# Optimization experiments

Hardware: AMD Instinct MI355X
Metric: run time of the kernel (lower is better)

## Reference

```python
import jax, jax.numpy as jnp
import numpy as np


def setup_inputs() -> dict:
    key = jax.random.key(0)
    ks = jax.random.split(key, 5)
    B, T, in_dim, out_dim = 8, 1024, 4096, 4096
    b_in, b_out, bs_in, bs_out, rank = 16, 16, 256, 256, 128
    std = np.sqrt(0.02).astype(np.float32)
    x = jax.random.normal(ks[0], (B, T, in_dim), dtype=jnp.float32)
    S = jax.random.uniform(ks[1], (b_out, b_in, rank), dtype=jnp.float32)
    U = std * jax.random.normal(ks[2], (b_out, rank, bs_out), dtype=jnp.float32)
    Vt = std * jax.random.normal(ks[3], (b_in, bs_in, rank), dtype=jnp.float32)
    bias = jax.random.normal(ks[4], (out_dim,), dtype=jnp.float32)
    return {"x": x, "S": S, "U": U, "Vt": Vt, "bias": bias}


def _blast_weight(S, U, Vt, in_dim):
    # Faithful to AbstractBlast.weight(eye(in_dim)): pass identity through the
    # block low-rank chain to materialize the dense weight W (in_dim, out_dim).
    b_in, bs_in, rank = Vt.shape
    I = jnp.eye(in_dim, dtype=Vt.dtype)
    # xp: (b_in, in_dim, bs_in) -- block-column slices of the identity
    xp = I.reshape(in_dim, b_in, bs_in).transpose(1, 0, 2)
    y = jnp.einsum('jms,jsr->jmr', xp, Vt)     # (b_in, in_dim, rank)
    z = jnp.einsum('jmr,ojr->omr', y, S)        # (b_out, in_dim, rank)
    out = jnp.einsum('omr,orp->omp', z, U)      # (b_out, in_dim, bs_out)
    W = out.transpose(1, 0, 2).reshape(in_dim, -1)  # (in_dim, out_dim)
    return W


def reference(x, S, U, Vt, bias):
    in_dim = x.shape[-1]
    X = x.reshape(-1, in_dim)                   # to2D
    W = _blast_weight(S, U, Vt, in_dim)
    out = bias + X @ W                          # addmm
    return out.reshape(*x.shape[:-1], -1)       # undo_to2D
```

## Files before the change

### kernel.cpp

```cpp
#include <hip/hip_runtime.h>
#include <hip/hip_bf16.h>


typedef __bf16 bf16x8 __attribute__((ext_vector_type(8)));
typedef __bf16 bf16x4 __attribute__((ext_vector_type(4)));
typedef float  f32x4  __attribute__((ext_vector_type(4)));

#define IN_DIM  4096
#define OUT_DIM 4096
#define NROWS   8192
#define BJ      16
#define BO      16
#define RANK    128

__device__ __forceinline__ bf16x4 cvt4(f32x4 v) {
  bf16x4 r;
  r[0] = (__bf16)v[0]; r[1] = (__bf16)v[1]; r[2] = (__bf16)v[2]; r[3] = (__bf16)v[3];
  return r;
}
__device__ __forceinline__ f32x4 lo4(bf16x8 v) {
  return (f32x4){(float)v[0], (float)v[1], (float)v[2], (float)v[3]};
}
__device__ __forceinline__ f32x4 hi4(bf16x8 v) {
  return (f32x4){(float)v[4], (float)v[5], (float)v[6], (float)v[7]};
}

__global__ __launch_bounds__(256) void prep_vtf(
    const float* __restrict__ Vt, __bf16* __restrict__ vtf)
{
  __shared__ float t[32 * 129];
  const int tid = threadIdx.x;
  const int j   = blockIdx.x >> 3;
  const int ks  = blockIdx.x & 7;

  #pragma unroll
  for (int it = 0; it < 4; ++it) {
    const int c  = tid + it * 256;
    const int sr = c >> 5, r4 = c & 31;
    const f32x4 v = *(const f32x4*)(Vt + ((size_t)(j * 256 + ks * 32 + sr)) * RANK + r4 * 4);
    t[sr * 129 + r4 * 4 + 0] = v[0];
    t[sr * 129 + r4 * 4 + 1] = v[1];
    t[sr * 129 + r4 * 4 + 2] = v[2];
    t[sr * 129 + r4 * 4 + 3] = v[3];
  }
  __syncthreads();

  const int lane = tid & 63;
  const int l = lane & 15, lh = lane >> 4;
  #pragma unroll
  for (int h = 0; h < 2; ++h) {
    const int rf = (tid >> 6) + h * 4;
    bf16x8 o8;
    #pragma unroll
    for (int e = 0; e < 8; ++e)
      o8[e] = (__bf16)t[(lh * 8 + e) * 129 + rf * 16 + l];
    *(bf16x8*)&vtf[(((size_t)(j * 8 + rf) * 8 + ks) * 64 + lane) * 8] = o8;
  }
}

__global__ __launch_bounds__(256) void prep_utf(
    const float* __restrict__ U, __bf16* __restrict__ utf)
{
  __shared__ float t[32 * 257];
  const int tid = threadIdx.x;
  const int o   = blockIdx.x >> 2;
  const int ks  = blockIdx.x & 3;

  #pragma unroll
  for (int it = 0; it < 8; ++it) {
    const int c  = tid + it * 256;
    const int rr = c >> 6, p4 = c & 63;
    const f32x4 v = *(const f32x4*)(U + ((size_t)(o * RANK + ks * 32 + rr)) * 256 + p4 * 4);
    t[rr * 257 + p4 * 4 + 0] = v[0];
    t[rr * 257 + p4 * 4 + 1] = v[1];
    t[rr * 257 + p4 * 4 + 2] = v[2];
    t[rr * 257 + p4 * 4 + 3] = v[3];
  }
  __syncthreads();

  const int lane = tid & 63;
  const int l = lane & 15, lh = lane >> 4;
  #pragma unroll
  for (int h = 0; h < 4; ++h) {
    const int pf = (tid >> 6) + h * 4;
    bf16x8 o8;
    #pragma unroll
    for (int e = 0; e < 8; ++e)
      o8[e] = (__bf16)t[(lh * 8 + e) * 257 + pf * 16 + l];
    *(bf16x8*)&utf[(((size_t)(o * 16 + pf) * 4 + ks) * 64 + lane) * 8] = o8;
  }
}

__global__ __launch_bounds__(256, 4) void k1_T(
    const float* __restrict__ x, const __bf16* __restrict__ vtf,
    __bf16* __restrict__ T)
{
  __shared__ __bf16 X_lds[64 * 256];

  const int tid  = threadIdx.x;
  const int lane = tid & 63;
  const int w    = tid >> 6;
  const int l15  = lane & 15;
  const int lhi  = lane >> 4;
  const int b    = blockIdx.x;
  const int j    = (b >> 3) & 15;
  const int mt   = (b & 7) * 16 + (b >> 7);
  const size_t rowbase = (size_t)mt * 64;

  #pragma unroll
  for (int i = 0; i < 16; ++i) {
    const int row = w * 16 + i;
    const f32x4 v = __builtin_nontemporal_load(
        (const f32x4*)(x + (rowbase + row) * IN_DIM + j * 256 + lane * 4));
    const int c = (lane >> 1) ^ (row & 15);
    *(bf16x4*)&X_lds[row * 256 + c * 8 + (lane & 1) * 4] = cvt4(v);
  }
  __syncthreads();

  f32x4 acc[2][4];
  #pragma unroll
  for (int a = 0; a < 2; ++a)
    #pragma unroll
    for (int c = 0; c < 4; ++c) acc[a][c] = (f32x4){0.f, 0.f, 0.f, 0.f};

  const __bf16* va = vtf + ((size_t)(j * 8 + w * 2) * 8) * 512 + lane * 8;
  #pragma unroll
  for (int ks = 0; ks < 8; ++ks) {
    bf16x8 bfr[4];
    #pragma unroll
    for (int nf = 0; nf < 4; ++nf) {
      const int c = (ks * 4 + lhi) ^ l15;
      bfr[nf] = *(const bf16x8*)&X_lds[(nf * 16 + l15) * 256 + c * 8];
    }
    const bf16x8 a0 = *(const bf16x8*)(va + (size_t)ks * 512);
    const bf16x8 a1 = *(const bf16x8*)(va + (size_t)(8 + ks) * 512);
    #pragma unroll
    for (int nf = 0; nf < 4; ++nf) {
      acc[0][nf] = __builtin_amdgcn_mfma_f32_16x16x32_bf16(a0, bfr[nf], acc[0][nf], 0, 0, 0);
      acc[1][nf] = __builtin_amdgcn_mfma_f32_16x16x32_bf16(a1, bfr[nf], acc[1][nf], 0, 0, 0);
    }
  }
  #pragma unroll
  for (int rfi = 0; rfi < 2; ++rfi)
    #pragma unroll
    for (int nf = 0; nf < 4; ++nf) {
      *(bf16x4*)&T[((size_t)j * NROWS + rowbase + nf * 16 + l15) * RANK
                   + (w * 2 + rfi) * 16 + lhi * 4] = cvt4(acc[rfi][nf]);
    }
}

__global__ __launch_bounds__(256, 4) void k2_fused(
    const __bf16* __restrict__ T, const float* __restrict__ S,
    const __bf16* __restrict__ utf, const float* __restrict__ bias,
    float* __restrict__ out)
{
  __shared__ __bf16 u_lds[64 * RANK];

  const int tid = threadIdx.x;
  const int b   = blockIdx.x;
  const int o   = (b >> 3) & 15;
  const int mt  = (b & 7) * 16 + (b >> 7);
  const size_t rowbase = (size_t)mt * 64;

  {
    const int nb = tid >> 4;
    const int rs = tid & 15;
    const __bf16* tg = T + (rowbase + nb * 4) * RANK + rs * 8;
    const float*  sp = S + (size_t)o * (BJ * RANK) + rs * 8;
    const size_t jstride = (size_t)NROWS * RANK;
    f32x4 uac[4][2];
    #pragma unroll
    for (int i = 0; i < 4; ++i) {
      uac[i][0] = (f32x4){0.f, 0.f, 0.f, 0.f};
      uac[i][1] = (f32x4){0.f, 0.f, 0.f, 0.f};
    }

    #pragma unroll 4
    for (int jb = 0; jb < BJ; ++jb) {
      const __bf16* tj = tg + (size_t)jb * jstride;
      bf16x8 tv[4];
      #pragma unroll
      for (int i = 0; i < 4; ++i) tv[i] = *(const bf16x8*)(tj + i * RANK);
      const f32x4 s0 = *(const f32x4*)(sp + jb * RANK);
      const f32x4 s1 = *(const f32x4*)(sp + jb * RANK + 4);
      #pragma unroll
      for (int i = 0; i < 4; ++i) {
        uac[i][0] = s0 * lo4(tv[i]) + uac[i][0];
        uac[i][1] = s1 * hi4(tv[i]) + uac[i][1];
      }
    }
    #pragma unroll
    for (int i = 0; i < 4; ++i) {
      const int n = nb * 4 + i;
      bf16x8 uw;
      const f32x4 a = uac[i][0], bb = uac[i][1];
      uw[0]=(__bf16)a[0];  uw[1]=(__bf16)a[1];  uw[2]=(__bf16)a[2];  uw[3]=(__bf16)a[3];
      uw[4]=(__bf16)bb[0]; uw[5]=(__bf16)bb[1]; uw[6]=(__bf16)bb[2]; uw[7]=(__bf16)bb[3];
      const int swz = rs ^ (n & 15);
      *(bf16x8*)&u_lds[n * RANK + swz * 8] = uw;
    }
  }
  __syncthreads();

  {
    const int lane = tid & 63;
    const int w    = tid >> 6;
    const int l15  = lane & 15;
    const int lhi  = lane >> 4;

    f32x4 acc[4][4];
    #pragma unroll
    for (int a = 0; a < 4; ++a)
      #pragma unroll
      for (int c = 0; c < 4; ++c) acc[a][c] = (f32x4){0.f, 0.f, 0.f, 0.f};

    #pragma unroll
    for (int ks = 0; ks < 4; ++ks) {
      bf16x8 ubf[4];
      #pragma unroll
      for (int nf = 0; nf < 4; ++nf) {
        const int swz = (ks * 4 + lhi) ^ l15;
        ubf[nf] = *(const bf16x8*)&u_lds[(nf * 16 + l15) * RANK + swz * 8];
      }
      #pragma unroll
      for (int pi = 0; pi < 4; ++pi) {
        const bf16x8 af = *(const bf16x8*)(
            utf + ((size_t)((o * 16 + w * 4 + pi) * 4 + ks)) * 512 + lane * 8);
        #pragma unroll
        for (int nf = 0; nf < 4; ++nf)
          acc[pi][nf] = __builtin_amdgcn_mfma_f32_16x16x32_bf16(af, ubf[nf], acc[pi][nf], 0, 0, 0);
      }
    }

    #pragma unroll
    for (int pi = 0; pi < 4; ++pi) {
      const int colb = o * 256 + (w * 4 + pi) * 16 + lhi * 4;
      const f32x4 bv = *(const f32x4*)(bias + colb);
      #pragma unroll
      for (int nf = 0; nf < 4; ++nf) {
        __builtin_nontemporal_store(acc[pi][nf] + bv,
            (f32x4*)(out + (rowbase + nf * 16 + l15) * OUT_DIM + colb));
      }
    }
  }
}

extern "C" void kernel_launch(void* const* d_in, const int* in_sizes, int n_in,
                              void* d_out, int out_size, void* d_ws, size_t ws_size,
                              hipStream_t stream) {
  const float* x    = (const float*)d_in[0];
  const float* S    = (const float*)d_in[1];
  const float* U    = (const float*)d_in[2];
  const float* Vt   = (const float*)d_in[3];
  const float* bias = (const float*)d_in[4];
  float* out = (float*)d_out;

  __bf16* vtf = (__bf16*)d_ws;
  __bf16* utf = vtf + (size_t)BJ * 8 * 8 * 512;
  __bf16* T   = utf + (size_t)BO * 16 * 4 * 512;

  prep_vtf<<<BJ * 8, 256, 0, stream>>>(Vt, vtf);
  prep_utf<<<BO * 4, 256, 0, stream>>>(U, utf);
  k1_T<<<(NROWS / 64) * BJ, 256, 0, stream>>>(x, vtf, T);
  k2_fused<<<(NROWS / 64) * BO, 256, 0, stream>>>(T, S, utf, bias, out);
}
```

Measured before the change: 103.7 us.

## Restructure k2 to stage all T blocks for 16 rows in LDS and loop over outputs

k2 now assigns each 512-thread workgroup 16 rows and stages T for all 16 input blocks into LDS once. It then loops over all 16 output blocks, computing the S-mixed intermediate into a double-buffered LDS tile and running a small MFMA against U, where before each workgroup re-read T from global memory for a single output block. k1 also stages its output through swizzled LDS so T is written with full-row coalesced stores. The new k2 uses small 16-row MFMA tiles with per-output synchronisation and reloads utf from global on every output iteration, which may lower MFMA efficiency and raise barrier overhead.

```diff
diff --git a/kernel.cpp b/kernel.cpp
--- a/kernel.cpp
+++ b/kernel.cpp
@@ -140,106 +140,94 @@
       acc[1][nf] = __builtin_amdgcn_mfma_f32_16x16x32_bf16(a1, bfr[nf], acc[1][nf], 0, 0, 0);
     }
   }
+  __syncthreads();
+
   #pragma unroll
   for (int rfi = 0; rfi < 2; ++rfi)
     #pragma unroll
     for (int nf = 0; nf < 4; ++nf) {
-      *(bf16x4*)&T[((size_t)j * NROWS + rowbase + nf * 16 + l15) * RANK
-                   + (w * 2 + rfi) * 16 + lhi * 4] = cvt4(acc[rfi][nf]);
-    }
-}
-
-__global__ __launch_bounds__(256, 4) void k2_fused(
+      const int n  = nf * 16 + l15;
+      const int c8 = (w * 2 + rfi) * 4 + lhi;
+      const int cs = c8 ^ ((n & 7) << 2);
+      *(bf16x4*)&X_lds[n * 128 + cs * 4] = cvt4(acc[rfi][nf]);
+    }
+  __syncthreads();
+
+  #pragma unroll
+  for (int i = 0; i < 4; ++i) {
+    const int row = w * 16 + i * 4 + (lane >> 4);
+    const int m   = lane & 15;
+    const int ms  = m ^ ((row & 7) << 1);
+    const bf16x8 v = *(const bf16x8*)&X_lds[row * 128 + ms * 8];
+    *(bf16x8*)&T[((size_t)j * NROWS + rowbase + row) * RANK + m * 8] = v;
+  }
+}
+
+__global__ __launch_bounds__(512, 2) void k2_fused(
     const __bf16* __restrict__ T, const float* __restrict__ S,
     const __bf16* __restrict__ utf, const float* __restrict__ bias,
     float* __restrict__ out)
 {
-  __shared__ __bf16 u_lds[64 * RANK];
-
-  const int tid = threadIdx.x;
-  const int b   = blockIdx.x;
-  const int o   = (b >> 3) & 15;
-  const int mt  = (b & 7) * 16 + (b >> 7);
-  const size_t rowbase = (size_t)mt * 64;
-
-  {
-    const int nb = tid >> 4;
-    const int rs = tid & 15;
-    const __bf16* tg = T + (rowbase + nb * 4) * RANK + rs * 8;
-    const float*  sp = S + (size_t)o * (BJ * RANK) + rs * 8;
-    const size_t jstride = (size_t)NROWS * RANK;
-    f32x4 uac[4][2];
-    #pragma unroll
-    for (int i = 0; i < 4; ++i) {
-      uac[i][0] = (f32x4){0.f, 0.f, 0.f, 0.f};
-      uac[i][1] = (f32x4){0.f, 0.f, 0.f, 0.f};
-    }
-
-    #pragma unroll 4
-    for (int jb = 0; jb < BJ; ++jb) {
-      const __bf16* tj = tg + (size_t)jb * jstride;
-      bf16x8 tv[4];
+  __shared__ __bf16 T_lds[BJ * 16 * RANK];
+  __shared__ __bf16 u_lds[2][16 * RANK];
+
+  const int tid  = threadIdx.x;
+  const int lane = tid & 63;
+  const int w    = tid >> 6;
+  const int l15  = lane & 15;
+  const int lhi  = lane >> 4;
+  const size_t rowbase = (size_t)blockIdx.x * 16;
+
+  #pragma unroll
+  for (int it = 0; it < 8; ++it) {
+    const int idx = it * 512 + tid;
+    const int j = idx >> 8, q = idx & 255;
+    const int n = q >> 4, m = q & 15;
+    const bf16x8 v = *(const bf16x8*)&T[((size_t)j * NROWS + rowbase + n) * RANK + m * 8];
+    *(bf16x8*)&T_lds[(j * 16 + n) * RANK + m * 8] = v;
+  }
+  __syncthreads();
+
+  const int fn = tid >> 5;
+  const int rs = tid & 31;
+
+  for (int o = 0; o < BO; ++o) {
+    {
+      f32x4 acc = {0.f, 0.f, 0.f, 0.f};
+      const float* sp = S + (size_t)o * (BJ * RANK) + rs * 4;
       #pragma unroll
-      for (int i = 0; i < 4; ++i) tv[i] = *(const bf16x8*)(tj + i * RANK);
-      const f32x4 s0 = *(const f32x4*)(sp + jb * RANK);
-      const f32x4 s1 = *(const f32x4*)(sp + jb * RANK + 4);
-      #pragma unroll
-      for (int i = 0; i < 4; ++i) {
-        uac[i][0] = s0 * lo4(tv[i]) + uac[i][0];
-        uac[i][1] = s1 * hi4(tv[i]) + uac[i][1];
+      for (int j = 0; j < BJ; ++j) {
+        const bf16x4 tv = *(const bf16x4*)&T_lds[(j * 16 + fn) * RANK + rs * 4];
+        const f32x4 sv = *(const f32x4*)(sp + j * RANK);
+        const f32x4 tf = {(float)tv[0], (float)tv[1], (float)tv[2], (float)tv[3]};
+        acc = sv * tf + acc;
       }
-    }
-    #pragma unroll
-    for (int i = 0; i < 4; ++i) {
-      const int n = nb * 4 + i;
-      bf16x8 uw;
-      const f32x4 a = uac[i][0], bb = uac[i][1];
-      uw[0]=(__bf16)a[0];  uw[1]=(__bf16)a[1];  uw[2]=(__bf16)a[2];  uw[3]=(__bf16)a[3];
-      uw[4]=(__bf16)bb[0]; uw[5]=(__bf16)bb[1]; uw[6]=(__bf16)bb[2]; uw[7]=(__bf16)bb[3];
-      const int swz = rs ^ (n & 15);
-      *(bf16x8*)&u_lds[n * RANK + swz * 8] = uw;
-    }
-  }
-  __syncthreads();
-
-  {
-    const int lane = tid & 63;
-    const int w    = tid >> 6;
-    const int l15  = lane & 15;
-    const int lhi  = lane >> 4;
-
-    f32x4 acc[4][4];
-    #pragma unroll
-    for (int a = 0; a < 4; ++a)
-      #pragma unroll
-      for (int c = 0; c < 4; ++c) acc[a][c] = (f32x4){0.f, 0.f, 0.f, 0.f};
-
-    #pragma unroll
-    for (int ks = 0; ks < 4; ++ks) {
+      const int c16 = rs >> 1, h = rs & 1;
+      const int cs  = c16 ^ fn;
+      *(bf16x4*)&u_lds[o & 1][fn * RANK + cs * 8 + h * 4] = cvt4(acc);
+    }
+    __syncthreads();
+
+    {
       bf16x8 ubf[4];
       #pragma unroll
-      for (int nf = 0; nf < 4; ++nf) {
-        const int swz = (ks * 4 + lhi) ^ l15;
-        ubf[nf] = *(const bf16x8*)&u_lds[(nf * 16 + l15) * RANK + swz * 8];
+      for (int ks = 0; ks < 4; ++ks) {
+        const int cs = (ks * 4 + lhi) ^ l15;
+        ubf[ks] = *(const bf16x8*)&u_lds[o & 1][l15 * RANK + cs * 8];
       }
       #pragma unroll
-      for (int pi = 0; pi < 4; ++pi) {
-        const bf16x8 af = *(const bf16x8*)(
-            utf + ((size_t)((o * 16 + w * 4 + pi) * 4 + ks)) * 512 + lane * 8);
+      for (int q = 0; q < 2; ++q) {
+        const int pf = w * 2 + q;
+        f32x4 acc = {0.f, 0.f, 0.f, 0.f};
+        const __bf16* uab = utf + ((size_t)((o * 16 + pf) * 4)) * 512 + lane * 8;
         #pragma unroll
-        for (int nf = 0; nf < 4; ++nf)
-          acc[pi][nf] = __builtin_amdgcn_mfma_f32_16x16x32_bf16(af, ubf[nf], acc[pi][nf], 0, 0, 0);
-      }
-    }
-
-    #pragma unroll
-    for (int pi = 0; pi < 4; ++pi) {
-      const int colb = o * 256 + (w * 4 + pi) * 16 + lhi * 4;
-      const f32x4 bv = *(const f32x4*)(bias + colb);
-      #pragma unroll
-      for (int nf = 0; nf < 4; ++nf) {
-        __builtin_nontemporal_store(acc[pi][nf] + bv,
-            (f32x4*)(out + (rowbase + nf * 16 + l15) * OUT_DIM + colb));
+        for (int ks = 0; ks < 4; ++ks) {
+          const bf16x8 af = *(const bf16x8*)(uab + (size_t)ks * 512);
+          acc = __builtin_amdgcn_mfma_f32_16x16x32_bf16(af, ubf[ks], acc, 0, 0, 0);
+        }
+        const int colb = o * 256 + pf * 16 + lhi * 4;
+        const f32x4 bv = *(const f32x4*)(bias + colb);
+        *(f32x4*)(out + (rowbase + l15) * OUT_DIM + colb) = acc + bv;
       }
     }
   }
@@ -262,5 +250,5 @@
   prep_vtf<<<BJ * 8, 256, 0, stream>>>(Vt, vtf);
   prep_utf<<<BO * 4, 256, 0, stream>>>(U, utf);
   k1_T<<<(NROWS / 64) * BJ, 256, 0, stream>>>(x, vtf, T);
-  k2_fused<<<(NROWS / 64) * BO, 256, 0, stream>>>(T, S, utf, bias, out);
-}
+  k2_fused<<<NROWS / 16, 512, 0, stream>>>(T, S, utf, bias, out);
+}
```

New measurement: 126.8 us. 22.3% more time.
